# Optimization experiments

Hardware: AMD Instinct MI355X
Metric: run time of the kernel (lower is better)

## Reference

```python
import jax, jax.numpy as jnp
import numpy as np
from jax import lax

BN_EPS = 1e-3  # keras BatchNormalization default epsilon
TOP_K = 2      # keep_top_k


def _conv3(x, k, b, s):
    # x: NDHWC, k: DHWIO, 'SAME' padding like keras Conv3D(padding='same')
    y = lax.conv_general_dilated(x, k, (s, s, s), 'SAME',
                                 dimension_numbers=('NDHWC', 'DHWIO', 'NDHWC'))
    return y + b


def _bn(x, g, be, m, v):
    # inference-mode batch norm with moving statistics
    return g * (x - m) * lax.rsqrt(v + BN_EPS) + be


def setup_inputs() -> dict:
    key = jax.random.key(0)
    ks = jax.random.split(key, 64)
    B, S = 16, 96
    nf, ksz, nE, nb = 32, 3, 8, 4
    inp = {"x": jax.random.normal(ks[0], (B, S, S, S, 1), jnp.float32)}
    cin = 1
    for i in range(nb):
        cout = nf * 2 ** i
        base = 1 + 6 * i
        inp["k%d" % i] = jax.random.normal(ks[base], (ksz, ksz, ksz, cin, cout), jnp.float32) * 0.05
        inp["b%d" % i] = jnp.zeros((cout,), jnp.float32)
        inp["g%d" % i] = 1.0 + 0.1 * jax.random.normal(ks[base + 1], (cout,), jnp.float32)
        inp["be%d" % i] = 0.1 * jax.random.normal(ks[base + 2], (cout,), jnp.float32)
        inp["m%d" % i] = 0.1 * jax.random.normal(ks[base + 3], (cout,), jnp.float32)
        inp["v%d" % i] = jax.random.uniform(ks[base + 4], (cout,), jnp.float32, 0.5, 1.5)
        cin = cout
    c = nf * 2 ** (nb - 1)  # 256
    inp["w1k"] = jax.random.normal(ks[30], (1, 1, 1, c, c), jnp.float32) * 0.05
    inp["w1b"] = jnp.zeros((c,), jnp.float32)
    inp["wg"] = 1.0 + 0.1 * jax.random.normal(ks[31], (c,), jnp.float32)
    inp["wbe"] = 0.1 * jax.random.normal(ks[32], (c,), jnp.float32)
    inp["wm"] = 0.1 * jax.random.normal(ks[33], (c,), jnp.float32)
    inp["wv"] = jax.random.uniform(ks[34], (c,), jnp.float32, 0.5, 1.5)
    inp["w2k"] = jax.random.normal(ks[35], (1, 1, 1, c, nE), jnp.float32) * 0.05
    inp["w2b"] = jnp.zeros((nE,), jnp.float32)
    return inp


def reference(x, k0, b0, g0, be0, m0, v0, k1, b1, g1, be1, m1, v1,
              k2, b2, g2, be2, m2, v2, k3, b3, g3, be3, m3, v3,
              w1k, w1b, wg, wbe, wm, wv, w2k, w2b):
    blocks = [(k0, b0, g0, be0, m0, v0), (k1, b1, g1, be1, m1, v1),
              (k2, b2, g2, be2, m2, v2), (k3, b3, g3, be3, m3, v3)]
    h = x
    for k, b, g, be, m, v in blocks:  # EncoderBlock: Conv3D(stride 2)+BN+ReLU
        h = jax.nn.relu(_bn(_conv3(h, k, b, 2), g, be, m, v))
    h = jnp.mean(h, axis=(1, 2, 3), keepdims=True)  # GAP, [B,1,1,1,256]
    w = _conv3(h, w1k, w1b, 1)
    w = jax.nn.relu(_bn(w, wg, wbe, wm, wv))
    w = _conv3(w, w2k, w2b, 1)  # [B,1,1,1,n_experts]
    # noisy-top-k gating (noise disabled at inference): mask non-top-k to -inf
    top_vals = lax.top_k(w, TOP_K)[0]
    thr = top_vals[..., TOP_K - 1:TOP_K]
    w = jnp.where(w >= thr, w, -jnp.inf)
    return jax.nn.softmax(w, axis=-1)
```

## Files before the change

### kernel.cpp

```cpp
#include <hip/hip_runtime.h>
#include <math.h>

#define BN_EPS 1e-3f

typedef __attribute__((ext_vector_type(8))) unsigned short ushort8v;
typedef __attribute__((ext_vector_type(8))) short short8v;
typedef __attribute__((ext_vector_type(4))) float f32x4;
typedef __attribute__((ext_vector_type(4))) unsigned int uint4v;

__device__ __forceinline__ float4 f4load(const float* p) {
    return *reinterpret_cast<const float4*>(p);
}
__device__ __forceinline__ float bf2f(unsigned short u) {
    union { unsigned int i; float f; } w; w.i = ((unsigned int)u) << 16; return w.f;
}
__device__ __forceinline__ unsigned short f2bf(float f) {
    union { float fv; unsigned int i; } w; w.fv = f;
    unsigned int lsb = (w.i >> 16) & 1u;
    w.i += 0x7fffu + lsb;
    return (unsigned short)(w.i >> 16);
}
__device__ __forceinline__ unsigned cvtpk(float lo, float hi) {
    unsigned r;
    asm("v_cvt_pk_bf16_f32 %0, %1, %2" : "=v"(r) : "v"(lo), "v"(hi));
    return r;
}
template<int N> __device__ __forceinline__ void waitv() {
    asm volatile("s_waitcnt vmcnt(%0)" :: "n"(N) : "memory");
}
__device__ __forceinline__ int xcd_swz(int bid, int nwg) {
    return (bid & 7) * (nwg >> 3) + (bid >> 3);
}

#define GLOAD_LDS16(g, l)                                                     \
    __builtin_amdgcn_global_load_lds(                                         \
        (const __attribute__((address_space(1))) void*)(const void*)(g),      \
        (__attribute__((address_space(3))) void*)(void*)(l), 16, 0, 0)

template<int CIN, int COUT>
__device__ __forceinline__ void wprep_body(
    const float* __restrict__ k, unsigned short* __restrict__ wt, int blk)
{
    constexpr int NS = COUT / 16;
    constexpr int KS = CIN / 32;
    int idx = blk * 256 + (int)threadIdx.x;
    if (idx >= 27 * KS * NS * 64) return;
    int lane = idx & 63;
    int nsg  = (idx >> 6) % NS;
    int it   = idx / (64 * NS);
    int tap  = it / KS;
    int ks   = it - tap * KS;
    int sg = lane >> 4, lr = lane & 15;
    int cout = nsg * 16 + lr;
    ushort8v o;
    #pragma unroll
    for (int j = 0; j < 8; ++j) {
        int ci = ks * 32 + sg * 8 + j;
        o[j] = f2bf(k[(size_t)(tap * CIN + ci) * COUT + cout]);
    }
    *reinterpret_cast<ushort8v*>(wt + (size_t)idx * 8) = o;
}

__global__ __launch_bounds__(256) void wprep_all(
    const float* __restrict__ k0,
    const float* __restrict__ k1, const float* __restrict__ k2, const float* __restrict__ k3,
    unsigned short* __restrict__ w0f,
    unsigned short* __restrict__ w1, unsigned short* __restrict__ w2, unsigned short* __restrict__ w3,
    unsigned short* __restrict__ zp)
{
    int b = blockIdx.x;
    if (b < 27)       wprep_body<32, 64>(k1, w1, b);
    else if (b < 135) wprep_body<64, 128>(k2, w2, b - 27);
    else if (b < 567) wprep_body<128, 256>(k3, w3, b - 135);
    else {
        reinterpret_cast<unsigned int*>(zp)[threadIdx.x] = 0u;
        {
            int t = (int)threadIdx.x;
            int lane = t & 63;
            int mf = (t >> 6) & 1;
            int ns = t >> 7;
            int sg = lane >> 4, lr = lane & 15;
            ushort8v o;
            #pragma unroll
            for (int j = 0; j < 8; ++j) {
                int jj = mf * 8 + j;
                bool valid = (sg < 3) && (jj < 9);
                int tap = sg * 9 + jj;
                o[j] = valid ? f2bf(k0[tap * 32 + ns * 16 + lr]) : (unsigned short)0;
            }
            *reinterpret_cast<ushort8v*>(w0f + (size_t)t * 8) = o;
        }
    }
}

__global__ __launch_bounds__(256) void conv0_lds(
    const float* __restrict__ x, const unsigned short* __restrict__ w0f,
    const float* __restrict__ zf,
    const float* __restrict__ b, const float* __restrict__ g,
    const float* __restrict__ be, const float* __restrict__ m,
    const float* __restrict__ v, unsigned short* __restrict__ y)
{
    __shared__ __attribute__((aligned(16))) float tile[81 * 36];

    const int l   = threadIdx.x & 63;
    const int wid = threadIdx.x >> 6;
    const int sg  = l >> 4;
    const int lr  = l & 15;

    int bb = xcd_swz(blockIdx.x, 6912);
    const int owt = bb % 3;  bb /= 3;
    const int oht = bb % 12; bb /= 12;
    const int odt = bb % 12; const int n = bb / 12;

    const int id0 = odt * 8, ih0 = oht * 8, iw0 = owt * 32;

    #pragma unroll
    for (int q0 = 0; q0 < 729; q0 += 256) {
        int qq = q0 + wid * 64;
        int q  = qq + l;
        if (qq < 729 && q < 729) {
            int row = q / 9, c = q - row * 9;
            int dd = row / 9, hh = row - dd * 9;
            int id = id0 + dd, ih = ih0 + hh;
            const float* src =
                (id < 96 && ih < 96 && (c < 8 || iw0 + 32 < 96))
                ? x + ((size_t)(n * 96 + id) * 96 + ih) * 96 + iw0 + c * 4
                : zf;
            GLOAD_LDS16(src, (char*)tile + (size_t)qq * 16);
        }
    }
    __syncthreads();

    const short8v B00 = *(const short8v*)(w0f + (size_t)(0 * 64 + l) * 8);
    const short8v B01 = *(const short8v*)(w0f + (size_t)(1 * 64 + l) * 8);
    const short8v B10 = *(const short8v*)(w0f + (size_t)(2 * 64 + l) * 8);
    const short8v B11 = *(const short8v*)(w0f + (size_t)(3 * 64 + l) * 8);

    float rc[9][3];
    {
        int dcl = (sg < 3) ? (2 * wid + sg) : 0;
        const float* rb = tile + (size_t)(dcl * 9) * 36 + 2 * lr;
        #pragma unroll
        for (int r = 0; r < 9; ++r) {
            float2 lo = *reinterpret_cast<const float2*>(rb + r * 36);
            rc[r][0] = lo.x; rc[r][1] = lo.y;
            rc[r][2] = rb[r * 36 + 2];
        }
    }

    f32x4 acc[4][2];
    #pragma unroll
    for (int mi = 0; mi < 4; ++mi) {
        acc[mi][0] = (f32x4){0.f, 0.f, 0.f, 0.f};
        acc[mi][1] = (f32x4){0.f, 0.f, 0.f, 0.f};
    }

    #pragma unroll
    for (int mi = 0; mi < 4; ++mi) {
        const int h0 = 2 * mi;
        uint4v au0;
        au0[0] = cvtpk(rc[h0][0],     rc[h0][1]);
        au0[1] = cvtpk(rc[h0][2],     rc[h0 + 1][0]);
        au0[2] = cvtpk(rc[h0 + 1][1], rc[h0 + 1][2]);
        au0[3] = cvtpk(rc[h0 + 2][0], rc[h0 + 2][1]);
        short8v a0 = __builtin_bit_cast(short8v, au0);
        uint4v au1;
        au1[0] = cvtpk(rc[h0 + 2][2], 0.f);
        au1[1] = 0; au1[2] = 0; au1[3] = 0;
        short8v a1 = __builtin_bit_cast(short8v, au1);
        acc[mi][0] = __builtin_amdgcn_mfma_f32_16x16x32_bf16(B00, a0, acc[mi][0], 0, 0, 0);
        acc[mi][0] = __builtin_amdgcn_mfma_f32_16x16x32_bf16(B01, a1, acc[mi][0], 0, 0, 0);
        acc[mi][1] = __builtin_amdgcn_mfma_f32_16x16x32_bf16(B10, a0, acc[mi][1], 0, 0, 0);
        acc[mi][1] = __builtin_amdgcn_mfma_f32_16x16x32_bf16(B11, a1, acc[mi][1], 0, 0, 0);
    }

    float4 Sv[2], Tv[2];
    #pragma unroll
    for (int ns = 0; ns < 2; ++ns) {
        int c0 = ns * 16 + sg * 4;
        float4 gv = f4load(g + c0), vv = f4load(v + c0);
        float4 bv = f4load(b + c0), mv = f4load(m + c0), bev = f4load(be + c0);
        Sv[ns].x = gv.x * rsqrtf(vv.x + BN_EPS);
        Sv[ns].y = gv.y * rsqrtf(vv.y + BN_EPS);
        Sv[ns].z = gv.z * rsqrtf(vv.z + BN_EPS);
        Sv[ns].w = gv.w * rsqrtf(vv.w + BN_EPS);
        Tv[ns].x = (bv.x - mv.x) * Sv[ns].x + bev.x;
        Tv[ns].y = (bv.y - mv.y) * Sv[ns].y + bev.y;
        Tv[ns].z = (bv.z - mv.z) * Sv[ns].z + bev.z;
        Tv[ns].w = (bv.w - mv.w) * Sv[ns].w + bev.w;
    }
    const int odG = odt * 4 + wid;
    const int owG = owt * 16 + lr;
    #pragma unroll
    for (int mi = 0; mi < 4; ++mi) {
        int oh = oht * 4 + mi;
        unsigned short* yp =
            y + (((size_t)(n * 48 + odG) * 48 + oh) * 48 + owG) * 32;
        #pragma unroll
        for (int ns = 0; ns < 2; ++ns) {
            float v0 = fmaxf(acc[mi][ns][0] * Sv[ns].x + Tv[ns].x, 0.f);
            float v1 = fmaxf(acc[mi][ns][1] * Sv[ns].y + Tv[ns].y, 0.f);
            float v2 = fmaxf(acc[mi][ns][2] * Sv[ns].z + Tv[ns].z, 0.f);
            float v3 = fmaxf(acc[mi][ns][3] * Sv[ns].w + Tv[ns].w, 0.f);
            uint2 uu;
            uu.x = cvtpk(v0, v1);
            uu.y = cvtpk(v2, v3);
            *reinterpret_cast<uint2*>(yp + ns * 16 + sg * 4) = uu;
        }
    }
}

template<int CIN, int COUT, int INS, int OUTS, int MW, int NSW, int NH,
         int CSPLIT, int KU, int NWG>
__global__ __launch_bounds__(256, 2) void conv_mfma_lds(
    const unsigned short* __restrict__ x, const unsigned short* __restrict__ wt,
    const unsigned short* __restrict__ zp,
    const float* __restrict__ b, const float* __restrict__ g,
    const float* __restrict__ be, const float* __restrict__ m,
    const float* __restrict__ v, unsigned short* __restrict__ y)
{
    constexpr int NSfull = COUT / 16;
    constexpr int NSB = NSW * NH;
    constexpr int KS = CIN / 32;
    constexpr int NITK = 27 * KS;
    constexpr int NIT = NITK / KU;
    constexpr int MGROUPS = 4 / NH;
    constexpr int MTILE = MGROUPS * MW * 16;
    constexpr int BSTEP = NSB * KU * 1024;
    constexpr int ASTEP = MGROUPS * MW * KU * 1024;
    constexpr int STRIDE = BSTEP + ASTEP;
    constexpr int BL = (NSB * KU) / 4;
    constexpr int AL = MW * KU;
    static_assert(NSB * CSPLIT == NSfull && NITK % KU == 0 && (NSB * KU) % 4 == 0, "tiling");
    static_assert(NIT >= 3, "pipeline depth");

    __shared__ __attribute__((aligned(16))) char lds[4 * STRIDE];

    const int l   = threadIdx.x & 63;
    const int wid = threadIdx.x >> 6;
    const int sg  = l >> 4;
    const int lr  = l & 15;

    const int sbid   = xcd_swz(blockIdx.x, NWG);
    const int mblk   = sbid / CSPLIT;
    const int cchunk = sbid % CSPLIT;
    const int mgroup = wid / NH;
    const int ngroup = wid % NH;
    const int gCoutBase = (cchunk * NSB + ngroup * NSW) * 16;
    const int vwave = mblk * MTILE + mgroup * MW * 16;

    const int vvS = l >> 2;
    const int ssS = ((l & 3) - (l >> 3)) & 3;

    const unsigned short* ap0[MW];
    unsigned smask[MW];
    #pragma unroll
    for (int mi = 0; mi < MW; ++mi) {
        int vA = vwave + mi * 16 + vvS;
        int owA = vA % OUTS; int t1 = vA / OUTS;
        int ohA = t1 % OUTS; int t2 = t1 / OUTS;
        int odA = t2 % OUTS; int nA = t2 / OUTS;
        ap0[mi] = x + ((((size_t)nA * INS + 2 * odA) * INS + 2 * ohA) * INS + 2 * owA) * CIN + ssS * 8;
        smask[mi] = ((odA == OUTS - 1) ? 0x07FC0000u : 0u)
                  | ((ohA == OUTS - 1) ? 0x070381C0u : 0u)
                  | ((owA == OUTS - 1) ? 0x04924924u : 0u);
    }

    const unsigned short* zpl = (const unsigned short*)((const char*)zp + l * 16);
    const int slotA = (lr * 4 + ((sg + (lr >> 1)) & 3)) * 16;

    f32x4 acc[MW][NSW];
    #pragma unroll
    for (int mi = 0; mi < MW; ++mi)
        #pragma unroll
        for (int ns = 0; ns < NSW; ++ns) acc[mi][ns] = (f32x4){0.f, 0.f, 0.f, 0.f};

    auto stage = [&](int ito, int p) {
        char* dst = &lds[p * STRIDE];
        #pragma unroll
        for (int c = 0; c < BL; ++c) {
            int idx  = c * 256 + (int)threadIdx.x;
            int lane = idx & 63;
            int sub  = idx >> 6;
            int u    = sub / NSB;
            int grp  = sub % NSB;
            int it   = ito * KU + u;
            const unsigned short* src =
                wt + ((size_t)(it * NSfull + cchunk * NSB + grp) * 64 + lane) * 8;
            GLOAD_LDS16(src, dst + sub * 1024);
        }
        if (ngroup == 0) {
            #pragma unroll
            for (int u = 0; u < KU; ++u) {
                int it = ito * KU + u;
                int tap = (KS == 1) ? it : it / KS;
                int ks  = (KS == 1) ? 0  : it - tap * KS;
                int kd = tap / 9, r9 = tap - kd * 9, kh = r9 / 3, kw = r9 - kh * 3;
                size_t aoff = (size_t)((kd * INS + kh) * INS + kw) * CIN + ks * 32;
                #pragma unroll
                for (int mi = 0; mi < MW; ++mi) {
                    const unsigned short* ga =
                        ((smask[mi] >> tap) & 1u) ? zpl : (ap0[mi] + aoff);
                    GLOAD_LDS16(ga, dst + BSTEP + ((mgroup * MW + mi) * KU + u) * 1024);
                }
            }
        }
    };

    auto computestep = [&](const char* buf) {
        #pragma unroll
        for (int u = 0; u < KU; ++u) {
            short8v Bf[NSW], Af[MW];
            #pragma unroll
            for (int ns = 0; ns < NSW; ++ns)
                Bf[ns] = *(const short8v*)(buf + (u * NSB + ngroup * NSW + ns) * 1024 + l * 16);
            #pragma unroll
            for (int mi = 0; mi < MW; ++mi)
                Af[mi] = *(const short8v*)(buf + BSTEP + ((mgroup * MW + mi) * KU + u) * 1024 + slotA);
            #pragma unroll
            for (int mi = 0; mi < MW; ++mi)
                #pragma unroll
                for (int ns = 0; ns < NSW; ++ns)
                    acc[mi][ns] = __builtin_amdgcn_mfma_f32_16x16x32_bf16(Bf[ns], Af[mi], acc[mi][ns], 0, 0, 0);
        }
    };

    stage(0, 0);
    stage(1, 1);
    stage(2, 2);
    #pragma unroll 1
    for (int ito = 0; ito < NIT - 2; ++ito) {
        if (ngroup == 0) waitv<2 * (BL + AL)>(); else waitv<2 * BL>();
        __builtin_amdgcn_s_barrier();
        asm volatile("" ::: "memory");
        if (ito + 3 < NIT) stage(ito + 3, (ito + 3) & 3);
        computestep(&lds[(ito & 3) * STRIDE]);
    }
    if (ngroup == 0) waitv<BL + AL>(); else waitv<BL>();
    __builtin_amdgcn_s_barrier();
    asm volatile("" ::: "memory");
    computestep(&lds[((NIT - 2) & 3) * STRIDE]);
    waitv<0>();
    __builtin_amdgcn_s_barrier();
    asm volatile("" ::: "memory");
    computestep(&lds[((NIT - 1) & 3) * STRIDE]);

    float4 Sv[NSW], Tv[NSW];
    #pragma unroll
    for (int ns = 0; ns < NSW; ++ns) {
        int c0 = gCoutBase + ns * 16 + sg * 4;
        float4 gv = f4load(g + c0), vv = f4load(v + c0);
        float4 bv = f4load(b + c0), mv = f4load(m + c0), bev = f4load(be + c0);
        Sv[ns].x = gv.x * rsqrtf(vv.x + BN_EPS);
        Sv[ns].y = gv.y * rsqrtf(vv.y + BN_EPS);
        Sv[ns].z = gv.z * rsqrtf(vv.z + BN_EPS);
        Sv[ns].w = gv.w * rsqrtf(vv.w + BN_EPS);
        Tv[ns].x = (bv.x - mv.x) * Sv[ns].x + bev.x;
        Tv[ns].y = (bv.y - mv.y) * Sv[ns].y + bev.y;
        Tv[ns].z = (bv.z - mv.z) * Sv[ns].z + bev.z;
        Tv[ns].w = (bv.w - mv.w) * Sv[ns].w + bev.w;
    }
    #pragma unroll
    for (int mi = 0; mi < MW; ++mi) {
        int vD = vwave + mi * 16 + lr;
        int ow = vD % OUTS; int u1 = vD / OUTS;
        int oh = u1 % OUTS; int u2 = u1 / OUTS;
        int od = u2 % OUTS; int n = u2 / OUTS;
        unsigned short* yp =
            y + ((((size_t)n * OUTS + od) * OUTS + oh) * OUTS + ow) * COUT + gCoutBase;
        #pragma unroll
        for (int ns = 0; ns < NSW; ++ns) {
            float v0 = fmaxf(acc[mi][ns][0] * Sv[ns].x + Tv[ns].x, 0.f);
            float v1 = fmaxf(acc[mi][ns][1] * Sv[ns].y + Tv[ns].y, 0.f);
            float v2 = fmaxf(acc[mi][ns][2] * Sv[ns].z + Tv[ns].z, 0.f);
            float v3 = fmaxf(acc[mi][ns][3] * Sv[ns].w + Tv[ns].w, 0.f);
            uint2 uu;
            uu.x = cvtpk(v0, v1);
            uu.y = cvtpk(v2, v3);
            *reinterpret_cast<uint2*>(yp + ns * 16 + sg * 4) = uu;
        }
    }
}

__global__ __launch_bounds__(256) void head_kernel(
    const unsigned short* __restrict__ x4,
    const float* __restrict__ w1k, const float* __restrict__ w1b,
    const float* __restrict__ wg,  const float* __restrict__ wbe,
    const float* __restrict__ wm,  const float* __restrict__ wv,
    const float* __restrict__ w2k, const float* __restrict__ w2b,
    float* __restrict__ out)
{
    __shared__ float part[8][256];
    __shared__ float h[256];
    __shared__ float r[256];
    __shared__ float logits[8];

    const int n = blockIdx.x;
    const int t = threadIdx.x;
    const int c8 = t & 31;
    const int pg = t >> 5;

    const unsigned short* xb = x4 + (size_t)n * 216 * 256 + c8 * 8;
    float s[8] = {0.f, 0.f, 0.f, 0.f, 0.f, 0.f, 0.f, 0.f};
    for (int i = pg; i < 216; i += 8) {
        ushort8v v8 = *reinterpret_cast<const ushort8v*>(xb + (size_t)i * 256);
        #pragma unroll
        for (int j = 0; j < 8; ++j) s[j] += bf2f(v8[j]);
    }
    #pragma unroll
    for (int j = 0; j < 8; ++j) part[pg][c8 * 8 + j] = s[j];
    __syncthreads();

    float a = 0.f;
    #pragma unroll
    for (int gi = 0; gi < 8; ++gi) a += part[gi][t];
    h[t] = a * (1.0f / 216.0f);
    __syncthreads();

    float acc = w1b[t];
    #pragma unroll 4
    for (int ci = 0; ci < 256; ++ci) acc += h[ci] * w1k[ci * 256 + t];
    float sc = wg[t] * rsqrtf(wv[t] + BN_EPS);
    acc = (acc - wm[t]) * sc + wbe[t];
    r[t] = fmaxf(acc, 0.f);
    __syncthreads();

    if (t < 8) {
        float a2 = w2b[t];
        for (int ci = 0; ci < 256; ++ci) a2 += r[ci] * w2k[ci * 8 + t];
        logits[t] = a2;
    }
    __syncthreads();

    if (t == 0) {
        float m1 = -INFINITY, m2 = -INFINITY;
        for (int e = 0; e < 8; ++e) {
            float val = logits[e];
            if (val > m1) { m2 = m1; m1 = val; }
            else if (val > m2) { m2 = val; }
        }
        float thr = m2;
        float ex[8]; float sum = 0.f;
        for (int e = 0; e < 8; ++e) {
            float val = (logits[e] >= thr) ? logits[e] : -INFINITY;
            ex[e] = expf(val - m1);
            sum += ex[e];
        }
        float inv = 1.0f / sum;
        for (int e = 0; e < 8; ++e) out[n * 8 + e] = ex[e] * inv;
    }
}

extern "C" void kernel_launch(void* const* d_in, const int* in_sizes, int n_in,
                              void* d_out, int out_size, void* d_ws, size_t ws_size,
                              hipStream_t stream) {
    const float* x   = (const float*)d_in[0];
    const float* k0  = (const float*)d_in[1];
    const float* b0  = (const float*)d_in[2];
    const float* g0  = (const float*)d_in[3];
    const float* be0 = (const float*)d_in[4];
    const float* m0  = (const float*)d_in[5];
    const float* v0  = (const float*)d_in[6];
    const float* k1  = (const float*)d_in[7];
    const float* b1  = (const float*)d_in[8];
    const float* g1  = (const float*)d_in[9];
    const float* be1 = (const float*)d_in[10];
    const float* m1  = (const float*)d_in[11];
    const float* v1  = (const float*)d_in[12];
    const float* k2  = (const float*)d_in[13];
    const float* b2  = (const float*)d_in[14];
    const float* g2  = (const float*)d_in[15];
    const float* be2 = (const float*)d_in[16];
    const float* m2  = (const float*)d_in[17];
    const float* v2  = (const float*)d_in[18];
    const float* k3  = (const float*)d_in[19];
    const float* b3  = (const float*)d_in[20];
    const float* g3  = (const float*)d_in[21];
    const float* be3 = (const float*)d_in[22];
    const float* m3  = (const float*)d_in[23];
    const float* v3  = (const float*)d_in[24];
    const float* w1k = (const float*)d_in[25];
    const float* w1b = (const float*)d_in[26];
    const float* wg  = (const float*)d_in[27];
    const float* wbe = (const float*)d_in[28];
    const float* wm  = (const float*)d_in[29];
    const float* wv  = (const float*)d_in[30];
    const float* w2k = (const float*)d_in[31];
    const float* w2b = (const float*)d_in[32];

    unsigned short* x1  = (unsigned short*)d_ws;
    unsigned short* x2  = x1 + 56623104;
    unsigned short* x3  = x2 + 14155776;
    unsigned short* x4  = x3 + 3538944;
    unsigned short* Wt1 = x4 + 884736;
    unsigned short* Wt2 = Wt1 + 55296;
    unsigned short* Wt3 = Wt2 + 221184;
    unsigned short* zp  = Wt3 + 884736;
    unsigned short* W0f = zp + 512;

    wprep_all<<<568, 256, 0, stream>>>(k0, k1, k2, k3, W0f, Wt1, Wt2, Wt3, zp);
    conv0_lds<<<6912, 256, 0, stream>>>(x, W0f, (const float*)zp, b0, g0, be0, m0, v0, x1);
    conv_mfma_lds<32, 64, 48, 24, 2, 4, 1, 1, 1, 1728><<<1728, 256, 0, stream>>>(x1, Wt1, zp, b1, g1, be1, m1, v1, x2);
    conv_mfma_lds<64, 128, 24, 12, 1, 4, 2, 1, 1, 864><<<864, 256, 0, stream>>>(x2, Wt2, zp, b2, g2, be2, m2, v2, x3);
    conv_mfma_lds<128, 256, 12, 6, 1, 1, 4, 4, 2, 864><<<864, 256, 0, stream>>>(x3, Wt3, zp, b3, g3, be3, m3, v3, x4);
    head_kernel<<<16, 256, 0, stream>>>(x4, w1k, w1b, wg, wbe, wm, wv, w2k, w2b, (float*)d_out);
}
```

Before: 171.1 us.

## Process two conv0 tiles per block with double-buffered async LDS staging

The first convolution kernel now handles two output tiles per workgroup. Both input tiles are issued as async global-to-LDS loads up front into two LDS buffers, and a partial vmcnt wait lets compute on the first tile overlap the second tile's loads. This halves the grid and amortizes weight and BN-parameter loads, in exchange for doubled LDS per block, which may reduce occupancy. Every lane now issues a load (a zero-buffer load where out of range) so the counted waits line up.

```diff
diff --git a/kernel.cpp b/kernel.cpp
--- a/kernel.cpp
+++ b/kernel.cpp
@@ -93,86 +93,26 @@
     }
 }
 
-__global__ __launch_bounds__(256) void conv0_lds(
+__global__ __launch_bounds__(256) void conv0_p2(
     const float* __restrict__ x, const unsigned short* __restrict__ w0f,
     const float* __restrict__ zf,
     const float* __restrict__ b, const float* __restrict__ g,
     const float* __restrict__ be, const float* __restrict__ m,
     const float* __restrict__ v, unsigned short* __restrict__ y)
 {
-    __shared__ __attribute__((aligned(16))) float tile[81 * 36];
+    __shared__ __attribute__((aligned(16))) float tile[2][3072];
 
     const int l   = threadIdx.x & 63;
     const int wid = threadIdx.x >> 6;
     const int sg  = l >> 4;
     const int lr  = l & 15;
 
-    int bb = xcd_swz(blockIdx.x, 6912);
-    const int owt = bb % 3;  bb /= 3;
-    const int oht = bb % 12; bb /= 12;
-    const int odt = bb % 12; const int n = bb / 12;
-
-    const int id0 = odt * 8, ih0 = oht * 8, iw0 = owt * 32;
-
-    #pragma unroll
-    for (int q0 = 0; q0 < 729; q0 += 256) {
-        int qq = q0 + wid * 64;
-        int q  = qq + l;
-        if (qq < 729 && q < 729) {
-            int row = q / 9, c = q - row * 9;
-            int dd = row / 9, hh = row - dd * 9;
-            int id = id0 + dd, ih = ih0 + hh;
-            const float* src =
-                (id < 96 && ih < 96 && (c < 8 || iw0 + 32 < 96))
-                ? x + ((size_t)(n * 96 + id) * 96 + ih) * 96 + iw0 + c * 4
-                : zf;
-            GLOAD_LDS16(src, (char*)tile + (size_t)qq * 16);
-        }
-    }
-    __syncthreads();
+    const int sbid = xcd_swz(blockIdx.x, 3456);
 
     const short8v B00 = *(const short8v*)(w0f + (size_t)(0 * 64 + l) * 8);
     const short8v B01 = *(const short8v*)(w0f + (size_t)(1 * 64 + l) * 8);
     const short8v B10 = *(const short8v*)(w0f + (size_t)(2 * 64 + l) * 8);
     const short8v B11 = *(const short8v*)(w0f + (size_t)(3 * 64 + l) * 8);
-
-    float rc[9][3];
-    {
-        int dcl = (sg < 3) ? (2 * wid + sg) : 0;
-        const float* rb = tile + (size_t)(dcl * 9) * 36 + 2 * lr;
-        #pragma unroll
-        for (int r = 0; r < 9; ++r) {
-            float2 lo = *reinterpret_cast<const float2*>(rb + r * 36);
-            rc[r][0] = lo.x; rc[r][1] = lo.y;
-            rc[r][2] = rb[r * 36 + 2];
-        }
-    }
-
-    f32x4 acc[4][2];
-    #pragma unroll
-    for (int mi = 0; mi < 4; ++mi) {
-        acc[mi][0] = (f32x4){0.f, 0.f, 0.f, 0.f};
-        acc[mi][1] = (f32x4){0.f, 0.f, 0.f, 0.f};
-    }
-
-    #pragma unroll
-    for (int mi = 0; mi < 4; ++mi) {
-        const int h0 = 2 * mi;
-        uint4v au0;
-        au0[0] = cvtpk(rc[h0][0],     rc[h0][1]);
-        au0[1] = cvtpk(rc[h0][2],     rc[h0 + 1][0]);
-        au0[2] = cvtpk(rc[h0 + 1][1], rc[h0 + 1][2]);
-        au0[3] = cvtpk(rc[h0 + 2][0], rc[h0 + 2][1]);
-        short8v a0 = __builtin_bit_cast(short8v, au0);
-        uint4v au1;
-        au1[0] = cvtpk(rc[h0 + 2][2], 0.f);
-        au1[1] = 0; au1[2] = 0; au1[3] = 0;
-        short8v a1 = __builtin_bit_cast(short8v, au1);
-        acc[mi][0] = __builtin_amdgcn_mfma_f32_16x16x32_bf16(B00, a0, acc[mi][0], 0, 0, 0);
-        acc[mi][0] = __builtin_amdgcn_mfma_f32_16x16x32_bf16(B01, a1, acc[mi][0], 0, 0, 0);
-        acc[mi][1] = __builtin_amdgcn_mfma_f32_16x16x32_bf16(B10, a0, acc[mi][1], 0, 0, 0);
-        acc[mi][1] = __builtin_amdgcn_mfma_f32_16x16x32_bf16(B11, a1, acc[mi][1], 0, 0, 0);
-    }
 
     float4 Sv[2], Tv[2];
     #pragma unroll
@@ -189,25 +129,104 @@
         Tv[ns].z = (bv.z - mv.z) * Sv[ns].z + bev.z;
         Tv[ns].w = (bv.w - mv.w) * Sv[ns].w + bev.w;
     }
-    const int odG = odt * 4 + wid;
-    const int owG = owt * 16 + lr;
-    #pragma unroll
-    for (int mi = 0; mi < 4; ++mi) {
-        int oh = oht * 4 + mi;
-        unsigned short* yp =
-            y + (((size_t)(n * 48 + odG) * 48 + oh) * 48 + owG) * 32;
-        #pragma unroll
-        for (int ns = 0; ns < 2; ++ns) {
-            float v0 = fmaxf(acc[mi][ns][0] * Sv[ns].x + Tv[ns].x, 0.f);
-            float v1 = fmaxf(acc[mi][ns][1] * Sv[ns].y + Tv[ns].y, 0.f);
-            float v2 = fmaxf(acc[mi][ns][2] * Sv[ns].z + Tv[ns].z, 0.f);
-            float v3 = fmaxf(acc[mi][ns][3] * Sv[ns].w + Tv[ns].w, 0.f);
-            uint2 uu;
-            uu.x = cvtpk(v0, v1);
-            uu.y = cvtpk(v2, v3);
-            *reinterpret_cast<uint2*>(yp + ns * 16 + sg * 4) = uu;
-        }
-    }
+
+    auto stage = [&](int tid, int p) {
+        int bb = tid;
+        int owt = bb % 3;  bb /= 3;
+        int oht = bb % 12; bb /= 12;
+        int odt = bb % 12; int n = bb / 12;
+        int id0 = odt * 8, ih0 = oht * 8, iw0 = owt * 32;
+        char* dst = (char*)tile[p];
+        #pragma unroll
+        for (int q0 = 0; q0 < 768; q0 += 256) {
+            int qq = q0 + wid * 64;
+            int q  = qq + l;
+            const float* src = zf;
+            if (q < 729) {
+                int row = q / 9, c = q - row * 9;
+                int dd = row / 9, hh = row - dd * 9;
+                int id = id0 + dd, ih = ih0 + hh;
+                if (id < 96 && ih < 96 && (c < 8 || iw0 + 32 < 96))
+                    src = x + ((size_t)(n * 96 + id) * 96 + ih) * 96 + iw0 + c * 4;
+            }
+            GLOAD_LDS16(src, dst + (size_t)qq * 16);
+        }
+    };
+
+    auto compute = [&](int tid, int p) {
+        int bb = tid;
+        int owt = bb % 3;  bb /= 3;
+        int oht = bb % 12; bb /= 12;
+        int odt = bb % 12; int n = bb / 12;
+
+        float rc[9][3];
+        {
+            int dcl = (sg < 3) ? (2 * wid + sg) : 0;
+            const float* rb = tile[p] + (size_t)(dcl * 9) * 36 + 2 * lr;
+            #pragma unroll
+            for (int r = 0; r < 9; ++r) {
+                float2 lo = *reinterpret_cast<const float2*>(rb + r * 36);
+                rc[r][0] = lo.x; rc[r][1] = lo.y;
+                rc[r][2] = rb[r * 36 + 2];
+            }
+        }
+
+        f32x4 acc[4][2];
+        #pragma unroll
+        for (int mi = 0; mi < 4; ++mi) {
+            acc[mi][0] = (f32x4){0.f, 0.f, 0.f, 0.f};
+            acc[mi][1] = (f32x4){0.f, 0.f, 0.f, 0.f};
+        }
+        #pragma unroll
+        for (int mi = 0; mi < 4; ++mi) {
+            const int h0 = 2 * mi;
+            uint4v au0;
+            au0[0] = cvtpk(rc[h0][0],     rc[h0][1]);
+            au0[1] = cvtpk(rc[h0][2],     rc[h0 + 1][0]);
+            au0[2] = cvtpk(rc[h0 + 1][1], rc[h0 + 1][2]);
+            au0[3] = cvtpk(rc[h0 + 2][0], rc[h0 + 2][1]);
+            short8v a0 = __builtin_bit_cast(short8v, au0);
+            uint4v au1;
+            au1[0] = cvtpk(rc[h0 + 2][2], 0.f);
+            au1[1] = 0; au1[2] = 0; au1[3] = 0;
+            short8v a1 = __builtin_bit_cast(short8v, au1);
+            acc[mi][0] = __builtin_amdgcn_mfma_f32_16x16x32_bf16(B00, a0, acc[mi][0], 0, 0, 0);
+            acc[mi][0] = __builtin_amdgcn_mfma_f32_16x16x32_bf16(B01, a1, acc[mi][0], 0, 0, 0);
+            acc[mi][1] = __builtin_amdgcn_mfma_f32_16x16x32_bf16(B10, a0, acc[mi][1], 0, 0, 0);
+            acc[mi][1] = __builtin_amdgcn_mfma_f32_16x16x32_bf16(B11, a1, acc[mi][1], 0, 0, 0);
+        }
+
+        const int odG = odt * 4 + wid;
+        const int owG = owt * 16 + lr;
+        #pragma unroll
+        for (int mi = 0; mi < 4; ++mi) {
+            int oh = oht * 4 + mi;
+            unsigned short* yp =
+                y + (((size_t)(n * 48 + odG) * 48 + oh) * 48 + owG) * 32;
+            #pragma unroll
+            for (int ns = 0; ns < 2; ++ns) {
+                float v0 = fmaxf(acc[mi][ns][0] * Sv[ns].x + Tv[ns].x, 0.f);
+                float v1 = fmaxf(acc[mi][ns][1] * Sv[ns].y + Tv[ns].y, 0.f);
+                float v2 = fmaxf(acc[mi][ns][2] * Sv[ns].z + Tv[ns].z, 0.f);
+                float v3 = fmaxf(acc[mi][ns][3] * Sv[ns].w + Tv[ns].w, 0.f);
+                uint2 uu;
+                uu.x = cvtpk(v0, v1);
+                uu.y = cvtpk(v2, v3);
+                *reinterpret_cast<uint2*>(yp + ns * 16 + sg * 4) = uu;
+            }
+        }
+    };
+
+    stage(2 * sbid, 0);
+    stage(2 * sbid + 1, 1);
+    waitv<3>();
+    __builtin_amdgcn_s_barrier();
+    asm volatile("" ::: "memory");
+    compute(2 * sbid, 0);
+    waitv<8>();
+    __builtin_amdgcn_s_barrier();
+    asm volatile("" ::: "memory");
+    compute(2 * sbid + 1, 1);
 }
 
 template<int CIN, int COUT, int INS, int OUTS, int MW, int NSW, int NH,
@@ -499,7 +518,7 @@
     unsigned short* W0f = zp + 512;
 
     wprep_all<<<568, 256, 0, stream>>>(k0, k1, k2, k3, W0f, Wt1, Wt2, Wt3, zp);
-    conv0_lds<<<6912, 256, 0, stream>>>(x, W0f, (const float*)zp, b0, g0, be0, m0, v0, x1);
+    conv0_p2<<<3456, 256, 0, stream>>>(x, W0f, (const float*)zp, b0, g0, be0, m0, v0, x1);
     conv_mfma_lds<32, 64, 48, 24, 2, 4, 1, 1, 1, 1728><<<1728, 256, 0, stream>>>(x1, Wt1, zp, b1, g1, be1, m1, v1, x2);
     conv_mfma_lds<64, 128, 24, 12, 1, 4, 2, 1, 1, 864><<<864, 256, 0, stream>>>(x2, Wt2, zp, b2, g2, be2, m2, v2, x3);
     conv_mfma_lds<128, 256, 12, 6, 1, 1, 4, 4, 2, 864><<<864, 256, 0, stream>>>(x3, Wt3, zp, b3, g3, be3, m3, v3, x4);
```

Result: no change. 168.0 us (-1.8%).
